# Kernel tuning notes

Hardware: AMD Instinct MI355X
Metric: run time of the kernel (lower is better)

The kernel has to match this reference:

```python
import jax, jax.numpy as jnp
import numpy as np

# Module config (matches init_kwargs)
N_HEADS = 16
HEAD = 64
SEQ = 4096          # single prefill sequence (cu_seqlens_k = [0, SEQ])
BS = 64             # block_size (both q and k blocks)
LOCAL = 8           # local_blocks
VERT = 8            # vert_stride
NB = SEQ // BS      # number of blocks along seq
SLIDE = max(1, VERT // N_HEADS)  # get_head_sliding_step(16, 8, homo_head=False) -> 1
SM_SCALE = 1.0 / float(np.sqrt(HEAD))


def _build_layout():
    """Per-head block-sparse layout: causal + (local OR strided-vertical) blocks,
    padded to a fixed max nnz per row (CSR rows -> padded col indices + valid mask)."""
    h = np.arange(N_HEADS)[:, None, None]
    i = np.arange(NB)[None, :, None]
    j = np.arange(NB)[None, None, :]
    mask = (j <= i) & (((i - j) < LOCAL) | (((j + h * SLIDE + 1) % VERT) == 0))
    max_nnz = int(mask.sum(-1).max())
    cols = np.zeros((N_HEADS, NB, max_nnz), np.int32)
    valid = np.zeros((N_HEADS, NB, max_nnz), bool)
    for hh in range(N_HEADS):
        for ii in range(NB):
            c = np.nonzero(mask[hh, ii])[0]
            cols[hh, ii, :len(c)] = c
            valid[hh, ii, :len(c)] = True
    return cols, valid, max_nnz

_COLS_NP, _VALID_NP, MAX_NNZ = _build_layout()
COLS = jnp.asarray(_COLS_NP)    # [H, NB, NNZ] k-block ids (padded with 0)
VALID = jnp.asarray(_VALID_NP)  # [H, NB, NNZ] padding mask


def setup_inputs() -> dict:
    key = jax.random.key(0)
    kq, kk, kv = jax.random.split(key, 3)
    q = jax.random.normal(kq, (SEQ, N_HEADS, HEAD), jnp.float32)
    k = jax.random.normal(kk, (SEQ, N_HEADS, HEAD), jnp.float32)
    v = jax.random.normal(kv, (SEQ, N_HEADS, HEAD), jnp.float32)
    cu_seqlens_k = jnp.array([0, SEQ], jnp.int32)
    return {"q": q, "k": k, "v": v, "cu_seqlens_k": cu_seqlens_k}


def _attn(q, k, v):
    # [T, H, D] -> [H, NB, BS, D]
    qb = q.transpose(1, 0, 2).reshape(N_HEADS, NB, BS, HEAD)
    kb = k.transpose(1, 0, 2).reshape(N_HEADS, NB, BS, HEAD)
    vb = v.transpose(1, 0, 2).reshape(N_HEADS, NB, BS, HEAD)
    gather = jax.vmap(lambda x, c: x[c])  # per-head block gather
    kg = gather(kb, COLS)  # [H, NB, NNZ, BS, D]
    vg = gather(vb, COLS)  # [H, NB, NNZ, BS, D]
    # block-sparse scores: [H, NB(q blk), BS(m), NNZ(n), BS(j)]
    scores = jnp.einsum('himd,hinjd->himnj', qb, kg) * SM_SCALE
    qpos = jnp.arange(NB)[:, None] * BS + jnp.arange(BS)[None, :]   # [NB, BS]
    kpos = COLS[..., None] * BS + jnp.arange(BS)                    # [H, NB, NNZ, BS]
    allow = VALID[:, :, None, :, None] & (
        qpos[None, :, :, None, None] >= kpos[:, :, None, :, :])
    scores = jnp.where(allow, scores, -jnp.inf)
    p = jax.nn.softmax(scores.reshape(N_HEADS, NB, BS, MAX_NNZ * BS), axis=-1)
    p = p.reshape(N_HEADS, NB, BS, MAX_NNZ, BS)
    out = jnp.einsum('himnj,hinjd->himd', p, vg)
    return out.reshape(N_HEADS, SEQ, HEAD).transpose(1, 0, 2)  # [T, H, D]


def reference(q, k, v, cu_seqlens_k):
    # single-sequence prefill: past_len = 0, q_len == k_len == SEQ
    return _attn(q, k, v)
```

## Files before the change

kernel.cpp:

```cpp
#include <hip/hip_runtime.h>
#include <hip/hip_bf16.h>
#include <math.h>


#define NHEADS 16
#define HDIM   64
#define NBLK   64
#define SEQLEN 4096
#define KP     72
#define SMAX   16.0f

typedef __attribute__((ext_vector_type(8))) short bf16x8;
typedef __attribute__((ext_vector_type(4))) float f32x4;

__device__ __forceinline__ short f2bf(float x) {
    union { float f; unsigned u; } c; c.f = x;
    unsigned u = c.u;
    return (short)((u + 0x7FFFu + ((u >> 16) & 1u)) >> 16);
}
__device__ __forceinline__ short f2bf_trunc(float x) {
    union { float f; unsigned u; } c; c.f = x;
    return (short)(c.u >> 16);
}

__device__ __forceinline__ void load_lds16(const short* g, const short* l) {
    __builtin_amdgcn_global_load_lds(
        (const __attribute__((address_space(1))) void*)g,
        (__attribute__((address_space(3))) void*)l, 16, 0, 0);
}

__global__ __launch_bounds__(256)
void prep_kernel(const float* __restrict__ k, const float* __restrict__ v,
                 short* __restrict__ kt, short* __restrict__ vt) {
    __shared__ short tile[64 * KP];
    const int b = blockIdx.x;
    const int h = b >> 6, jb = b & 63;
    const int tid = threadIdx.x;

    {
        const int kg = tid >> 4;
        const int dg = tid & 15;
        float4 f[4];
        #pragma unroll
        for (int j = 0; j < 4; ++j)
            f[j] = *(const float4*)(v + ((size_t)(jb * 64 + 4 * kg + j) * NHEADS + h) * HDIM + 4 * dg);
        #pragma unroll
        for (int i = 0; i < 4; ++i) {
            short4 s4;
            s4.x = f2bf(((const float*)&f[0])[i]);
            s4.y = f2bf(((const float*)&f[1])[i]);
            s4.z = f2bf(((const float*)&f[2])[i]);
            s4.w = f2bf(((const float*)&f[3])[i]);
            *(short4*)&tile[(4 * dg + i) * KP + 4 * kg] = s4;
        }
    }
    __syncthreads();
    short* vtile = vt + (size_t)b * 4096;
    #pragma unroll
    for (int ii = 0; ii < 2; ++ii) {
        int idx = ii * 256 + tid;
        int d = idx >> 3, gsw = idx & 7;
        int g = gsw ^ (d & 7);
        bf16x8 val = *(const bf16x8*)&tile[d * KP + g * 8];
        *(bf16x8*)(vtile + (size_t)idx * 8) = val;
    }
    short* ktile = kt + (size_t)b * 4096;
    #pragma unroll
    for (int ii = 0; ii < 2; ++ii) {
        int idx = ii * 256 + tid;
        int r = idx >> 3, g = idx & 7;
        const float* src = k + ((size_t)(jb * 64 + r) * NHEADS + h) * HDIM + g * 8;
        float4 f0 = *(const float4*)src;
        float4 f1 = *(const float4*)(src + 4);
        bf16x8 a;
        a[0]=f2bf(f0.x); a[1]=f2bf(f0.y); a[2]=f2bf(f0.z); a[3]=f2bf(f0.w);
        a[4]=f2bf(f1.x); a[5]=f2bf(f1.y); a[6]=f2bf(f1.z); a[7]=f2bf(f1.w);
        int G = r * 8 + (g ^ (r & 7));
        *(bf16x8*)(ktile + (size_t)G * 8) = a;
    }
}

__global__ __launch_bounds__(256, 4)
void attn_kernel(const short* __restrict__ kt, const short* __restrict__ vt,
                 const float* __restrict__ q, float* __restrict__ out) {
    __shared__ short kl[2 * 4096];
    __shared__ short pl[4 * 1024];

    const int b    = blockIdx.x;
    const int h    = ((b & 7) << 1) | ((b >> 3) & 1);
    const int g6   = b >> 4;
    const int qi   = (g6 & 1) ? (63 - (g6 >> 1)) : (g6 >> 1);
    const int tid  = threadIdx.x;
    const int wave = tid >> 6;
    const int lane = tid & 63;
    const int l16  = lane & 15;
    const int quad = lane >> 4;
    const int row0 = qi * 64 + wave * 16;
    short* pw = pl + wave * 1024;

    const float* qrow = q + ((size_t)(row0 + l16) * NHEADS + h) * HDIM;
    bf16x8 a_q[2];
    #pragma unroll
    for (int kk = 0; kk < 2; ++kk) {
        const float* src = qrow + kk * 32 + quad * 8;
        float4 f0 = *(const float4*)(src);
        float4 f1 = *(const float4*)(src + 4);
        bf16x8 a;
        a[0]=f2bf(f0.x); a[1]=f2bf(f0.y); a[2]=f2bf(f0.z); a[3]=f2bf(f0.w);
        a[4]=f2bf(f1.x); a[5]=f2bf(f1.y); a[6]=f2bf(f1.z); a[7]=f2bf(f1.w);
        a_q[kk] = a;
    }

    f32x4 o[4];
    float lsum[4];
    #pragma unroll
    for (int nt = 0; nt < 4; ++nt) { o[nt] = (f32x4){0.f,0.f,0.f,0.f}; lsum[nt] = 0.f; }

    const short* kth = kt + (size_t)(h * 64) * 4096;
    const short* vth = vt + (size_t)(h * 64) * 4096;
    const float kscale = 0.125f * 1.4426950408889634f;

    const int j0  = (7 - h) & 7;
    const int loc = (qi > 7) ? (qi - 7) : 0;
    const int nv  = (j0 < loc) ? ((loc - j0 + 7) >> 3) : 0;
    const int T   = nv + (qi - loc + 1);

    const int sbase = wave * 64;
    const int r7    = l16 & 7;
    const int gk0   = (quad ^ r7) * 8;
    const int gk1   = gk0 ^ 32;
    const int rowb  = l16 * 64;
    int vo[4][2];
    #pragma unroll
    for (int nt = 0; nt < 4; ++nt) {
        vo[nt][0] = (nt * 16 + l16) * 64 + gk0;
        vo[nt][1] = (nt * 16 + l16) * 64 + gk1;
    }
    const int pr0   = rowb + ((quad ^ r7) << 3);
    const int pr1   = rowb + (((4 + quad) ^ r7) << 3);

    {
        const short* ktb = kth + (size_t)((0 < nv) ? j0 : loc) * 4096;
        load_lds16(ktb + (size_t)(sbase + lane) * 8,       &kl[sbase * 8]);
        load_lds16(ktb + (size_t)(256 + sbase + lane) * 8, &kl[(256 + sbase) * 8]);
    }

    for (int t = 0; t < T; ++t) {
        const int jb = (t < nv) ? (j0 + 8 * t) : (loc + (t - nv));

        __syncthreads();

        if (t + 1 < T) {
            const int jn = (t + 1 < nv) ? (j0 + 8 * (t + 1)) : (loc + (t + 1 - nv));
            const int bo = ((t + 1) & 1) * 4096;
            const short* ktb = kth + (size_t)jn * 4096;
            load_lds16(ktb + (size_t)(sbase + lane) * 8,       &kl[bo + sbase * 8]);
            load_lds16(ktb + (size_t)(256 + sbase + lane) * 8, &kl[bo + (256 + sbase) * 8]);
        }

        const short* vtb = vth + (size_t)jb * 4096;
        bf16x8 vf[4][2];
        #pragma unroll
        for (int nt = 0; nt < 4; ++nt) {
            vf[nt][0] = *(const bf16x8*)(vtb + vo[nt][0]);
            vf[nt][1] = *(const bf16x8*)(vtb + vo[nt][1]);
        }

        const short* kb = &kl[(t & 1) * 4096];

        f32x4 s[4];
        #pragma unroll
        for (int nt = 0; nt < 4; ++nt) {
            bf16x8 k0 = *(const bf16x8*)&kb[nt * 1024 + rowb + gk0];
            bf16x8 k1 = *(const bf16x8*)&kb[nt * 1024 + rowb + gk1];
            s[nt] = (f32x4){0.f,0.f,0.f,0.f};
            s[nt] = __builtin_amdgcn_mfma_f32_16x16x32_bf16(a_q[0], k0, s[nt], 0, 0, 0);
            s[nt] = __builtin_amdgcn_mfma_f32_16x16x32_bf16(a_q[1], k1, s[nt], 0, 0, 0);
        }

        const bool diag = (jb == qi);
        #pragma unroll
        for (int nt = 0; nt < 4; ++nt) {
            const int gw = nt * 2 + (l16 >> 3);
            const int ow = l16 & 7;
            #pragma unroll
            for (int r = 0; r < 4; ++r) {
                float raw = s[nt][r];
                if (diag) {
                    int n = nt * 16 + l16;
                    int mrow = wave * 16 + quad * 4 + r;
                    if (n > mrow) raw = -INFINITY;
                }
                float pv = __builtin_amdgcn_exp2f(fmaf(raw, kscale, -SMAX));
                lsum[r] += pv;
                const int prow = quad * 4 + r;
                pw[prow * 64 + ((gw ^ (prow & 7)) << 3) + ow] = f2bf_trunc(pv);
            }
        }

        bf16x8 a_p0 = *(const bf16x8*)&pw[pr0];
        bf16x8 a_p1 = *(const bf16x8*)&pw[pr1];

        #pragma unroll
        for (int nt = 0; nt < 4; ++nt) {
            o[nt] = __builtin_amdgcn_mfma_f32_16x16x32_bf16(a_p0, vf[nt][0], o[nt], 0, 0, 0);
            o[nt] = __builtin_amdgcn_mfma_f32_16x16x32_bf16(a_p1, vf[nt][1], o[nt], 0, 0, 0);
        }
    }

    #pragma unroll
    for (int r = 0; r < 4; ++r) {
        float tsum = lsum[r];
        #pragma unroll
        for (int off = 1; off < 16; off <<= 1)
            tsum += __shfl_xor(tsum, off);
        float inv = 1.0f / tsum;
        int trow = row0 + quad * 4 + r;
        float* orow = out + ((size_t)trow * NHEADS + h) * HDIM;
        #pragma unroll
        for (int nt = 0; nt < 4; ++nt)
            orow[nt * 16 + l16] = o[nt][r] * inv;
    }
}

extern "C" void kernel_launch(void* const* d_in, const int* in_sizes, int n_in,
                              void* d_out, int out_size, void* d_ws, size_t ws_size,
                              hipStream_t stream) {
    const float* q = (const float*)d_in[0];
    const float* k = (const float*)d_in[1];
    const float* v = (const float*)d_in[2];
    float* out = (float*)d_out;

    const size_t tileBytes = (size_t)NHEADS * NBLK * 4096 * sizeof(short);
    short* kt = (short*)d_ws;
    short* vt = (short*)((char*)d_ws + tileBytes);
    prep_kernel<<<dim3(NHEADS * NBLK), dim3(256), 0, stream>>>(k, v, kt, vt);
    attn_kernel<<<dim3(NHEADS * NBLK), dim3(256), 0, stream>>>(kt, vt, q, out);
}
```

Baseline: 122.7 us.

## Software-pipeline QK scores one step ahead with triple-buffered K tiles

Moves to a three-slot LDS ring for K tiles with a prefetch distance of two, and computes the QK^T scores for the next block during the current iteration, between the softmax/P write and the PV MFMAs. The aim is to overlap the score MFMAs with the exp and LDS-store work and to hide global-to-LDS latency. In exchange it uses more LDS and more registers for the s_next accumulators, which may reduce occupancy under launch_bounds(256,4). There is also no explicit vmcnt wait on the async LDS loads before they are read, so correctness relies on the __syncthreads ordering.

```diff
diff --git a/kernel.cpp b/kernel.cpp
--- a/kernel.cpp
+++ b/kernel.cpp
@@ -83,7 +83,7 @@
 __global__ __launch_bounds__(256, 4)
 void attn_kernel(const short* __restrict__ kt, const short* __restrict__ vt,
                  const float* __restrict__ q, float* __restrict__ out) {
-    __shared__ short kl[2 * 4096];
+    __shared__ short kl[3 * 4096];
     __shared__ short pl[4 * 1024];
 
     const int b    = blockIdx.x;
@@ -124,6 +124,7 @@
     const int loc = (qi > 7) ? (qi - 7) : 0;
     const int nv  = (j0 < loc) ? ((loc - j0 + 7) >> 3) : 0;
     const int T   = nv + (qi - loc + 1);
+#define JB(u) (((u) < nv) ? (j0 + 8 * (u)) : (loc + ((u) - nv)))
 
     const int sbase = wave * 64;
     const int r7    = l16 & 7;
@@ -140,22 +141,37 @@
     const int pr1   = rowb + (((4 + quad) ^ r7) << 3);
 
     {
-        const short* ktb = kth + (size_t)((0 < nv) ? j0 : loc) * 4096;
-        load_lds16(ktb + (size_t)(sbase + lane) * 8,       &kl[sbase * 8]);
-        load_lds16(ktb + (size_t)(256 + sbase + lane) * 8, &kl[(256 + sbase) * 8]);
+        const short* k0 = kth + (size_t)JB(0) * 4096;
+        load_lds16(k0 + (size_t)(sbase + lane) * 8,       &kl[sbase * 8]);
+        load_lds16(k0 + (size_t)(256 + sbase + lane) * 8, &kl[(256 + sbase) * 8]);
+        if (1 < T) {
+            const short* k1 = kth + (size_t)JB(1) * 4096;
+            load_lds16(k1 + (size_t)(sbase + lane) * 8,       &kl[4096 + sbase * 8]);
+            load_lds16(k1 + (size_t)(256 + sbase + lane) * 8, &kl[4096 + (256 + sbase) * 8]);
+        }
+    }
+    __syncthreads();
+
+    f32x4 s_cur[4], s_next[4];
+    #pragma unroll
+    for (int nt = 0; nt < 4; ++nt) {
+        bf16x8 k0 = *(const bf16x8*)&kl[nt * 1024 + rowb + gk0];
+        bf16x8 k1 = *(const bf16x8*)&kl[nt * 1024 + rowb + gk1];
+        s_cur[nt] = (f32x4){0.f,0.f,0.f,0.f};
+        s_cur[nt] = __builtin_amdgcn_mfma_f32_16x16x32_bf16(a_q[0], k0, s_cur[nt], 0, 0, 0);
+        s_cur[nt] = __builtin_amdgcn_mfma_f32_16x16x32_bf16(a_q[1], k1, s_cur[nt], 0, 0, 0);
     }
 
     for (int t = 0; t < T; ++t) {
-        const int jb = (t < nv) ? (j0 + 8 * t) : (loc + (t - nv));
+        const int jb = JB(t);
 
         __syncthreads();
 
-        if (t + 1 < T) {
-            const int jn = (t + 1 < nv) ? (j0 + 8 * (t + 1)) : (loc + (t + 1 - nv));
-            const int bo = ((t + 1) & 1) * 4096;
-            const short* ktb = kth + (size_t)jn * 4096;
-            load_lds16(ktb + (size_t)(sbase + lane) * 8,       &kl[bo + sbase * 8]);
-            load_lds16(ktb + (size_t)(256 + sbase + lane) * 8, &kl[bo + (256 + sbase) * 8]);
+        if (t + 2 < T) {
+            const int so = ((t + 2) % 3) * 4096;
+            const short* kn = kth + (size_t)JB(t + 2) * 4096;
+            load_lds16(kn + (size_t)(sbase + lane) * 8,       &kl[so + sbase * 8]);
+            load_lds16(kn + (size_t)(256 + sbase + lane) * 8, &kl[so + (256 + sbase) * 8]);
         }
 
         const short* vtb = vth + (size_t)jb * 4096;
@@ -164,18 +180,6 @@
         for (int nt = 0; nt < 4; ++nt) {
             vf[nt][0] = *(const bf16x8*)(vtb + vo[nt][0]);
             vf[nt][1] = *(const bf16x8*)(vtb + vo[nt][1]);
-        }
-
-        const short* kb = &kl[(t & 1) * 4096];
-
-        f32x4 s[4];
-        #pragma unroll
-        for (int nt = 0; nt < 4; ++nt) {
-            bf16x8 k0 = *(const bf16x8*)&kb[nt * 1024 + rowb + gk0];
-            bf16x8 k1 = *(const bf16x8*)&kb[nt * 1024 + rowb + gk1];
-            s[nt] = (f32x4){0.f,0.f,0.f,0.f};
-            s[nt] = __builtin_amdgcn_mfma_f32_16x16x32_bf16(a_q[0], k0, s[nt], 0, 0, 0);
-            s[nt] = __builtin_amdgcn_mfma_f32_16x16x32_bf16(a_q[1], k1, s[nt], 0, 0, 0);
         }
 
         const bool diag = (jb == qi);
@@ -185,7 +189,7 @@
             const int ow = l16 & 7;
             #pragma unroll
             for (int r = 0; r < 4; ++r) {
-                float raw = s[nt][r];
+                float raw = s_cur[nt][r];
                 if (diag) {
                     int n = nt * 16 + l16;
                     int mrow = wave * 16 + quad * 4 + r;
@@ -198,6 +202,18 @@
             }
         }
 
+        if (t + 1 < T) {
+            const short* kb = &kl[((t + 1) % 3) * 4096];
+            #pragma unroll
+            for (int nt = 0; nt < 4; ++nt) {
+                bf16x8 k0 = *(const bf16x8*)&kb[nt * 1024 + rowb + gk0];
+                bf16x8 k1 = *(const bf16x8*)&kb[nt * 1024 + rowb + gk1];
+                s_next[nt] = (f32x4){0.f,0.f,0.f,0.f};
+                s_next[nt] = __builtin_amdgcn_mfma_f32_16x16x32_bf16(a_q[0], k0, s_next[nt], 0, 0, 0);
+                s_next[nt] = __builtin_amdgcn_mfma_f32_16x16x32_bf16(a_q[1], k1, s_next[nt], 0, 0, 0);
+            }
+        }
+
         bf16x8 a_p0 = *(const bf16x8*)&pw[pr0];
         bf16x8 a_p1 = *(const bf16x8*)&pw[pr1];
 
@@ -206,6 +222,9 @@
             o[nt] = __builtin_amdgcn_mfma_f32_16x16x32_bf16(a_p0, vf[nt][0], o[nt], 0, 0, 0);
             o[nt] = __builtin_amdgcn_mfma_f32_16x16x32_bf16(a_p1, vf[nt][1], o[nt], 0, 0, 0);
         }
+
+        #pragma unroll
+        for (int nt = 0; nt < 4; ++nt) s_cur[nt] = s_next[nt];
     }
 
     #pragma unroll
@@ -221,6 +240,7 @@
         for (int nt = 0; nt < 4; ++nt)
             orow[nt * 16 + l16] = o[nt][r] * inv;
     }
+#undef JB
 }
 
 extern "C" void kernel_launch(void* const* d_in, const int* in_sizes, int n_in,
```

Measured after the change: 128.4 us. 4.6% more time.
